# Performance work log

Measured on AMD Instinct MI355X. Metric: run time of the kernel, lower is better.

The kernel has to match this reference:

```python
import jax, jax.numpy as jnp
import numpy as np

N_HEAD = 16


def setup_inputs() -> dict:
    key = jax.random.key(0)
    ks = jax.random.split(key, 6)
    B, T, C = 2, 2048, 1024
    hs = C // N_HEAD  # 64
    block_minus_1 = 2048  # block_size - 1
    x = jax.random.normal(ks[0], (B, T, C), dtype=jnp.float32)
    W1 = jax.random.normal(ks[1], (C, C), dtype=jnp.float32) * (1.0 / np.sqrt(C))
    b1 = jnp.zeros((C,), dtype=jnp.float32)
    # original init: uniform(-1e-3, 1e-3)
    w2 = jax.random.uniform(ks[2], (hs, block_minus_1), dtype=jnp.float32, minval=-1e-3, maxval=1e-3)
    b2 = jnp.zeros((block_minus_1,), dtype=jnp.float32)
    Wv = jax.random.normal(ks[3], (C, C), dtype=jnp.float32) * (1.0 / np.sqrt(C))
    bv = jnp.zeros((C,), dtype=jnp.float32)
    Wp = jax.random.normal(ks[4], (C, C), dtype=jnp.float32) * (1.0 / np.sqrt(C))
    bp = jnp.zeros((C,), dtype=jnp.float32)
    return {"x": x, "W1": W1, "b1": b1, "w2": w2, "b2": b2,
            "Wv": Wv, "bv": bv, "Wp": Wp, "bp": bp}


def reference(x, W1, b1, w2, b2, Wv, bv, Wp, bp):
    B, T, C = x.shape
    hs = C // N_HEAD
    r = jax.nn.relu(x @ W1.T + b1).reshape(B, T, N_HEAD, hs).transpose(0, 2, 1, 3)
    # synthesizer scores: (B, nh, T, T) = relu_out @ w2[:, :T] + b2[:T]
    att = jnp.einsum('bhtd,dj->bhtj', r, w2[:, :T]) + b2[:T]
    causal = jnp.tril(jnp.ones((T, T), dtype=bool))
    att = jnp.where(causal[None, None], att, jnp.float32(-1e10))
    att = jax.nn.softmax(att, axis=-1)  # attn_drop = 0 (eval)
    v = (x @ Wv.T + bv).reshape(B, T, N_HEAD, hs).transpose(0, 2, 1, 3)
    y = jnp.einsum('bhtj,bhjd->bhtd', att, v)
    y = y.transpose(0, 2, 1, 3).reshape(B, T, C)
    return y @ Wp.T + bp  # resid_drop = 0 (eval)
```

## Files before the change

kernel.cpp:

```cpp
#include <hip/hip_runtime.h>

typedef __bf16 bf16x8 __attribute__((ext_vector_type(8)));
typedef float f32x4 __attribute__((ext_vector_type(4)));
typedef float f32x16 __attribute__((ext_vector_type(16)));

__device__ __forceinline__ unsigned short f2bf(float f) {
  union { float f; unsigned u; } v; v.f = f;
  unsigned u = v.u;
  return (unsigned short)((u + 0x7fffu + ((u >> 16) & 1u)) >> 16);
}
__device__ __forceinline__ void gload_lds16(const void* g, void* l) {
  __builtin_amdgcn_global_load_lds(
      (const __attribute__((address_space(1))) unsigned int*)g,
      (__attribute__((address_space(3))) unsigned int*)l, 16, 0, 0);
}
__device__ __forceinline__ unsigned cvtpk(float lo, float hi) {
  unsigned r;
  asm("v_cvt_pk_bf16_f32 %0, %1, %2" : "=v"(r) : "v"(lo), "v"(hi));
  return r;
}
__device__ __forceinline__ void cvt4(const float* __restrict__ s,
                                     unsigned short* __restrict__ d, int u) {
  f32x4 v = ((const f32x4*)s)[u];
  union { unsigned short s[4]; unsigned long long u; } o;
  o.s[0] = f2bf(v[0]); o.s[1] = f2bf(v[1]); o.s[2] = f2bf(v[2]); o.s[3] = f2bf(v[3]);
  ((unsigned long long*)d)[u] = o.u;
}


__global__ void prep(const float* __restrict__ x, const float* __restrict__ W1,
                     const float* __restrict__ Wv, const float* __restrict__ Wp,
                     const float* __restrict__ w2, const float* __restrict__ b2,
                     unsigned short* __restrict__ xb, unsigned short* __restrict__ W1b,
                     unsigned short* __restrict__ Wvb, unsigned short* __restrict__ Wpb,
                     unsigned short* __restrict__ w2t, unsigned short* __restrict__ ebj) {
  int u = blockIdx.x * 256 + threadIdx.x;
  if (u < 1048576) { cvt4(x, xb, u); return; }
  u -= 1048576;
  if (u < 262144) { cvt4(W1, W1b, u); return; }
  u -= 262144;
  if (u < 262144) { cvt4(Wv, Wvb, u); return; }
  u -= 262144;
  if (u < 262144) { cvt4(Wp, Wpb, u); return; }
  u -= 262144;
  if (u < 32768) {
    int j = u >> 4, d4 = (u & 15) * 4;
    union { unsigned short s[4]; unsigned long long x; } o;
#pragma unroll
    for (int i = 0; i < 4; ++i) o.s[i] = f2bf(w2[(d4 + i) * 2048 + j]);
    ((unsigned long long*)w2t)[u] = o.x;
    return;
  }
  u -= 32768;
  union { unsigned short s[4]; unsigned long long x; } o;
#pragma unroll
  for (int i = 0; i < 4; ++i) o.s[i] = f2bf(__expf(b2[u * 4 + i]));
  ((unsigned long long*)ebj)[u] = o.x;
}

__global__ __launch_bounds__(256, 3) void gemm_rv(
    const unsigned short* __restrict__ xb, const unsigned short* __restrict__ W1b,
    const unsigned short* __restrict__ Wvb, const float* __restrict__ b1,
    const float* __restrict__ bv, const float* __restrict__ b2,
    unsigned short* __restrict__ rb, unsigned short* __restrict__ vtb) {
  __shared__ unsigned short Xs[2][64 * 64];
  __shared__ unsigned short W1s[2][64 * 64];
  __shared__ unsigned short Wvs[2][64 * 64];
  const int tm = blockIdx.x * 64, n0 = blockIdx.y * 64;
  const int tid = threadIdx.x;
  const int wv = tid >> 6, ln = tid & 63;
  const int l5 = ln >> 5, l31 = ln & 31;
  const int tw = (wv & 1) * 32;
  const int cw = (wv >> 1) * 32;
  const int rowL = ln >> 3;
  const int kc = (((ln & 7) ^ rowL) & 7) * 8;

  int xoff[4], woff[4];
#pragma unroll
  for (int kk = 0; kk < 4; ++kk) {
    int c = kk * 2 + l5;
    int p = (c ^ (l31 & 7)) * 8;
    xoff[kk] = (tw + l31) * 64 + p;
    woff[kk] = (cw + l31) * 64 + p;
  }

  auto stage = [&](int k0, int bi) {
#pragma unroll
    for (int l = 0; l < 2; ++l) {
      int row = l * 32 + wv * 8 + rowL;
      gload_lds16(xb + (tm + row) * 1024 + k0 + kc, &Xs[bi][l * 2048 + wv * 512]);
      gload_lds16(W1b + (n0 + row) * 1024 + k0 + kc, &W1s[bi][l * 2048 + wv * 512]);
      gload_lds16(Wvb + (n0 + row) * 1024 + k0 + kc, &Wvs[bi][l * 2048 + wv * 512]);
    }
  };

  f32x16 accR, accV;
#pragma unroll
  for (int i = 0; i < 16; ++i) { accR[i] = 0.f; accV[i] = 0.f; }

  stage(0, 0);
  for (int it = 0; it < 16; ++it) {
    const int cb = it & 1;
    __syncthreads();
    if (it < 15) stage((it + 1) * 64, cb ^ 1);
#pragma unroll
    for (int kk = 0; kk < 4; ++kk) {
      bf16x8 xa  = *(const bf16x8*)&Xs[cb][xoff[kk]];
      bf16x8 w1f = *(const bf16x8*)&W1s[cb][woff[kk]];
      bf16x8 wvf = *(const bf16x8*)&Wvs[cb][woff[kk]];
      accR = __builtin_amdgcn_mfma_f32_32x32x16_bf16(xa, w1f, accR, 0, 0, 0);
      accV = __builtin_amdgcn_mfma_f32_32x32x16_bf16(wvf, xa, accV, 0, 0, 0);
    }
  }
  {
    int col = n0 + cw + l31;
    float bc = b1[col];
#pragma unroll
    for (int r = 0; r < 16; ++r) {
      int rr = (r & 3) + 8 * (r >> 2) + 4 * l5;
      float v = accR[r] + bc;
      rb[(tm + tw + rr) * 1024 + col] = f2bf(v > 0.f ? v : 0.f);
    }
  }
  {
    int tok = tm + tw + l31;
    float eb = __expf(b2[tok & 2047]);
#pragma unroll
    for (int r = 0; r < 16; ++r) {
      int rr = (r & 3) + 8 * (r >> 2) + 4 * l5;
      int ch = n0 + cw + rr;
      vtb[ch * 4096 + tok] = f2bf((accV[r] + bv[ch]) * eb);
    }
  }
}

__global__ __launch_bounds__(256, 4) void gemm_p(
    const unsigned short* __restrict__ A, const unsigned short* __restrict__ Bt,
    const float* __restrict__ bias, float* __restrict__ C) {
  __shared__ unsigned short As[2][64 * 64];
  __shared__ unsigned short Bs[2][64 * 64];
  const int tid = threadIdx.x;
  const int wv = tid >> 6, ln = tid & 63;
  const int l5 = ln >> 5, l31 = ln & 31;
  const int wm = (wv & 1) * 32, wn = (wv >> 1) * 32;
  const int tileM = blockIdx.y * 64, tileN = blockIdx.x * 64;
  const int rowL = ln >> 3;
  const int kc = (((ln & 7) ^ rowL) & 7) * 8;

  int aoff[4], boff[4];
#pragma unroll
  for (int kk = 0; kk < 4; ++kk) {
    int c = kk * 2 + l5;
    int p = (c ^ (l31 & 7)) * 8;
    aoff[kk] = (wm + l31) * 64 + p;
    boff[kk] = (wn + l31) * 64 + p;
  }

  auto stage = [&](int k0, int bi) {
#pragma unroll
    for (int l = 0; l < 2; ++l) {
      int row = l * 32 + wv * 8 + rowL;
      gload_lds16(A + (tileM + row) * 1024 + k0 + kc, &As[bi][l * 2048 + wv * 512]);
      gload_lds16(Bt + (tileN + row) * 1024 + k0 + kc, &Bs[bi][l * 2048 + wv * 512]);
    }
  };

  f32x16 acc;
#pragma unroll
  for (int i = 0; i < 16; ++i) acc[i] = 0.f;

  stage(0, 0);
  for (int it = 0; it < 16; ++it) {
    const int cb = it & 1;
    __syncthreads();
    if (it < 15) stage((it + 1) * 64, cb ^ 1);
#pragma unroll
    for (int kk = 0; kk < 4; ++kk) {
      bf16x8 af  = *(const bf16x8*)&As[cb][aoff[kk]];
      bf16x8 bfr = *(const bf16x8*)&Bs[cb][boff[kk]];
      acc = __builtin_amdgcn_mfma_f32_32x32x16_bf16(af, bfr, acc, 0, 0, 0);
    }
  }
#pragma unroll
  for (int r = 0; r < 16; ++r) {
    int rr = (r & 3) + 8 * (r >> 2) + 4 * l5;
    int row = tileM + wm + rr;
    int col = tileN + wn + l31;
    C[row * 1024 + col] = acc[r] + bias[col];
  }
}

__global__ __launch_bounds__(256, 2) void attn(
    const unsigned short* __restrict__ r, const unsigned short* __restrict__ w2t,
    const unsigned short* __restrict__ vt, const unsigned short* __restrict__ ebj,
    unsigned short* __restrict__ y) {
  __shared__ unsigned short W2s[2][64 * 64];
  __shared__ unsigned short Vs[2][64 * 64];

  const int tid = threadIdx.x;
  const int wv = tid >> 6, ln = tid & 63;
  const int quad = ln >> 4, lq = ln & 15;
  const int bh = blockIdx.x, b = bh >> 4, h = bh & 15;
  const int q = blockIdx.y;
  const int p = (q < 8) ? q : 23 - q;
  const int ta = p, tb = 31 - p;
  const int t0a = ta * 64, t0b = tb * 64;
  const int rowL = ln >> 3;
  const int kc = (((ln & 7) ^ rowL) & 7) * 8;
  const int sx = lq & 7;
  const int ko0 = (quad ^ sx) * 8, ko1 = ((4 + quad) ^ sx) * 8;

  bf16x8 ra[2][2];
  {
    const unsigned short* base = r + (b * 2048 + wv * 16 + lq) * 1024 + h * 64 + quad * 8;
    ra[0][0] = *(const bf16x8*)(base + t0a * 1024);
    ra[0][1] = *(const bf16x8*)(base + t0a * 1024 + 32);
    ra[1][0] = *(const bf16x8*)(base + t0b * 1024);
    ra[1][1] = *(const bf16x8*)(base + t0b * 1024 + 32);
  }

  f32x4 accY[2][4];
  f32x4 accL[2];
  const f32x4 zf = {0.f, 0.f, 0.f, 0.f};
#pragma unroll
  for (int s = 0; s < 2; ++s) {
    accL[s] = zf;
#pragma unroll
    for (int nd = 0; nd < 4; ++nd) accY[s][nd] = zf;
  }

  auto stage = [&](int jt, int bi) {
    int j0 = jt * 64;
#pragma unroll
    for (int l = 0; l < 2; ++l) {
      int row = l * 32 + wv * 8 + rowL;
      gload_lds16(w2t + (j0 + row) * 64 + kc, &W2s[bi][l * 2048 + wv * 512]);
      gload_lds16(vt + (h * 64 + row) * 4096 + b * 2048 + j0 + kc,
                  &Vs[bi][l * 2048 + wv * 512]);
    }
  };

#define TILE(S, T0, TT)                                                         \
    {                                                                           \
      f32x4 sv[4];                                                              \
      _Pragma("unroll") for (int ni = 0; ni < 4; ++ni) {                        \
        sv[ni] = __builtin_amdgcn_mfma_f32_16x16x32_bf16(w2f0[ni], ra[S][0], zf, 0, 0, 0); \
        sv[ni] = __builtin_amdgcn_mfma_f32_16x16x32_bf16(w2f1[ni], ra[S][1], sv[ni], 0, 0, 0); \
      }                                                                         \
      const bool diag = (jt == (TT));                                           \
      const int tl = (T0) + wv * 16 + lq;                                       \
      _Pragma("unroll") for (int ni = 0; ni < 4; ++ni)                          \
        _Pragma("unroll") for (int rg = 0; rg < 4; ++rg) {                      \
          float pe = __expf(sv[ni][rg]);                                        \
          if (diag) {                                                           \
            int j = j0 + ni * 16 + quad * 4 + rg;                               \
            pe = (j <= tl) ? pe : 0.f;                                          \
          }                                                                     \
          sv[ni][rg] = pe;                                                      \
        }                                                                       \
      bf16x8 pa0, pa1;                                                          \
      {                                                                         \
        union { unsigned u[4]; bf16x8 v; } k0u, k1u;                            \
        _Pragma("unroll") for (int pr = 0; pr < 2; ++pr) {                      \
          unsigned a0 = cvtpk(sv[0][2 * pr], sv[0][2 * pr + 1]);                \
          unsigned b0 = cvtpk(sv[1][2 * pr], sv[1][2 * pr + 1]);                \
          asm("v_permlane32_swap_b32 %0, %1" : "+v"(a0), "+v"(b0));             \
          asm("v_permlane16_swap_b32 %0, %1" : "+v"(a0), "+v"(b0));             \
          k0u.u[pr] = a0; k0u.u[2 + pr] = b0;                                   \
          unsigned a1 = cvtpk(sv[2][2 * pr], sv[2][2 * pr + 1]);                \
          unsigned b1 = cvtpk(sv[3][2 * pr], sv[3][2 * pr + 1]);                \
          asm("v_permlane32_swap_b32 %0, %1" : "+v"(a1), "+v"(b1));             \
          asm("v_permlane16_swap_b32 %0, %1" : "+v"(a1), "+v"(b1));             \
          k1u.u[pr] = a1; k1u.u[2 + pr] = b1;                                   \
        }                                                                       \
        pa0 = k0u.v; pa1 = k1u.v;                                               \
      }                                                                         \
      _Pragma("unroll") for (int nd = 0; nd < 4; ++nd) {                        \
        bf16x8 bb0 = *(const bf16x8*)&Vs[cb][(nd * 16 + lq) * 64 + ko0];        \
        accY[S][nd] = __builtin_amdgcn_mfma_f32_16x16x32_bf16(pa0, bb0, accY[S][nd], 0, 0, 0); \
        bf16x8 bb1 = *(const bf16x8*)&Vs[cb][(nd * 16 + lq) * 64 + ko1];        \
        accY[S][nd] = __builtin_amdgcn_mfma_f32_16x16x32_bf16(pa1, bb1, accY[S][nd], 0, 0, 0); \
      }                                                                         \
      accL[S] = __builtin_amdgcn_mfma_f32_16x16x32_bf16(pa0, eb0, accL[S], 0, 0, 0); \
      accL[S] = __builtin_amdgcn_mfma_f32_16x16x32_bf16(pa1, eb1, accL[S], 0, 0, 0); \
    }

#define WRITEOUT(S, T0)                                                         \
    {                                                                           \
      float inv[4];                                                             \
      _Pragma("unroll") for (int rg = 0; rg < 4; ++rg)                          \
        inv[rg] = __builtin_amdgcn_rcpf(accL[S][rg]);                           \
      _Pragma("unroll") for (int nd = 0; nd < 4; ++nd)                          \
        _Pragma("unroll") for (int rg = 0; rg < 4; ++rg) {                      \
          int t = (T0) + wv * 16 + quad * 4 + rg;                               \
          y[(b * 2048 + t) * 1024 + h * 64 + nd * 16 + lq] =                    \
              f2bf(accY[S][nd][rg] * inv[rg]);                                  \
        }                                                                       \
    }

  stage(0, 0);
  for (int jt = 0; jt <= tb; ++jt) {
    const int cb = jt & 1;
    __syncthreads();
    if (jt < tb) stage(jt + 1, cb ^ 1);
    const int j0 = jt * 64;

    bf16x8 eb0 = *(const bf16x8*)&ebj[j0 + quad * 8];
    bf16x8 eb1 = *(const bf16x8*)&ebj[j0 + 32 + quad * 8];
    bf16x8 w2f0[4], w2f1[4];
#pragma unroll
    for (int ni = 0; ni < 4; ++ni) {
      w2f0[ni] = *(const bf16x8*)&W2s[cb][(ni * 16 + lq) * 64 + ko0];
      w2f1[ni] = *(const bf16x8*)&W2s[cb][(ni * 16 + lq) * 64 + ko1];
    }

    if (jt <= ta) TILE(0, t0a, ta);
    TILE(1, t0b, tb);
    if (jt == ta) WRITEOUT(0, t0a);
  }
  WRITEOUT(1, t0b);
#undef TILE
#undef WRITEOUT
}

extern "C" void kernel_launch(void* const* d_in, const int* in_sizes, int n_in,
                              void* d_out, int out_size, void* d_ws, size_t ws_size,
                              hipStream_t stream) {
  const float* x  = (const float*)d_in[0];
  const float* W1 = (const float*)d_in[1];
  const float* b1 = (const float*)d_in[2];
  const float* w2 = (const float*)d_in[3];
  const float* b2 = (const float*)d_in[4];
  const float* Wv = (const float*)d_in[5];
  const float* bv = (const float*)d_in[6];
  const float* Wp = (const float*)d_in[7];
  const float* bp = (const float*)d_in[8];

  unsigned short* ws  = (unsigned short*)d_ws;
  unsigned short* xb   = ws;
  unsigned short* W1b  = ws + 4194304;
  unsigned short* Wvb  = ws + 5242880;
  unsigned short* Wpb  = ws + 6291456;
  unsigned short* w2t  = ws + 7340032;
  unsigned short* rb   = ws + 7471104;
  unsigned short* vt   = ws + 11665408;
  unsigned short* yb   = ws + 15859712;
  unsigned short* ebjb = ws + 20054016;

  prep<<<7298, 256, 0, stream>>>(x, W1, Wv, Wp, w2, b2, xb, W1b, Wvb, Wpb, w2t, ebjb);
  gemm_rv<<<dim3(64, 16), 256, 0, stream>>>(xb, W1b, Wvb, b1, bv, b2, rb, vt);
  attn<<<dim3(32, 16), 256, 0, stream>>>(rb, w2t, vt, ebjb, yb);
  gemm_p<<<dim3(16, 64), 256, 0, stream>>>(yb, Wpb, bp, (float*)d_out);
}
```

Measured before the change: 185.3 us.

## Triple-buffer LDS staging with explicit vmcnt waits in GEMM and attention kernels

Moves the GEMM and attention kernels from double-buffered LDS staging with __syncthreads to triple buffering. The prefetch now runs two tiles ahead, and each iteration waits only on its own tile through a partial s_waitcnt vmcnt plus a raw s_barrier, so one tile's loads stay in flight across the barrier. The aim is to hide more global-to-LDS latency behind the MFMA work. In exchange, LDS use per block grows and launch-bounds occupancy targets drop by one block per CU. The hand-written vmcnt counts must match the exact number of loads each stage issues.

Measured after the change: 168.7 us. -9.0%, faster.

```diff
diff --git a/kernel.cpp b/kernel.cpp
--- a/kernel.cpp
+++ b/kernel.cpp
@@ -18,6 +18,11 @@
   unsigned r;
   asm("v_cvt_pk_bf16_f32 %0, %1, %2" : "=v"(r) : "v"(lo), "v"(hi));
   return r;
+}
+template <int N> __device__ __forceinline__ void vmwait() {
+  if constexpr (N == 0) asm volatile("s_waitcnt vmcnt(0)" ::: "memory");
+  else if constexpr (N == 4) asm volatile("s_waitcnt vmcnt(4)" ::: "memory");
+  else asm volatile("s_waitcnt vmcnt(6)" ::: "memory");
 }
 __device__ __forceinline__ void cvt4(const float* __restrict__ s,
                                      unsigned short* __restrict__ d, int u) {
@@ -58,14 +63,14 @@
   ((unsigned long long*)ebj)[u] = o.x;
 }
 
-__global__ __launch_bounds__(256, 3) void gemm_rv(
+__global__ __launch_bounds__(256, 2) void gemm_rv(
     const unsigned short* __restrict__ xb, const unsigned short* __restrict__ W1b,
     const unsigned short* __restrict__ Wvb, const float* __restrict__ b1,
     const float* __restrict__ bv, const float* __restrict__ b2,
     unsigned short* __restrict__ rb, unsigned short* __restrict__ vtb) {
-  __shared__ unsigned short Xs[2][64 * 64];
-  __shared__ unsigned short W1s[2][64 * 64];
-  __shared__ unsigned short Wvs[2][64 * 64];
+  __shared__ unsigned short Xs[3][64 * 64];
+  __shared__ unsigned short W1s[3][64 * 64];
+  __shared__ unsigned short Wvs[3][64 * 64];
   const int tm = blockIdx.x * 64, n0 = blockIdx.y * 64;
   const int tid = threadIdx.x;
   const int wv = tid >> 6, ln = tid & 63;
@@ -99,10 +104,13 @@
   for (int i = 0; i < 16; ++i) { accR[i] = 0.f; accV[i] = 0.f; }
 
   stage(0, 0);
+  stage(64, 1);
   for (int it = 0; it < 16; ++it) {
-    const int cb = it & 1;
-    __syncthreads();
-    if (it < 15) stage((it + 1) * 64, cb ^ 1);
+    const int cb = it % 3;
+    if (it < 15) vmwait<6>(); else vmwait<0>();
+    __builtin_amdgcn_s_barrier();
+    __builtin_amdgcn_sched_barrier(0);
+    if (it < 14) stage((it + 2) * 64, (it + 2) % 3);
 #pragma unroll
     for (int kk = 0; kk < 4; ++kk) {
       bf16x8 xa  = *(const bf16x8*)&Xs[cb][xoff[kk]];
@@ -134,11 +142,11 @@
   }
 }
 
-__global__ __launch_bounds__(256, 4) void gemm_p(
+__global__ __launch_bounds__(256, 3) void gemm_p(
     const unsigned short* __restrict__ A, const unsigned short* __restrict__ Bt,
     const float* __restrict__ bias, float* __restrict__ C) {
-  __shared__ unsigned short As[2][64 * 64];
-  __shared__ unsigned short Bs[2][64 * 64];
+  __shared__ unsigned short As[3][64 * 64];
+  __shared__ unsigned short Bs[3][64 * 64];
   const int tid = threadIdx.x;
   const int wv = tid >> 6, ln = tid & 63;
   const int l5 = ln >> 5, l31 = ln & 31;
@@ -170,10 +178,13 @@
   for (int i = 0; i < 16; ++i) acc[i] = 0.f;
 
   stage(0, 0);
+  stage(64, 1);
   for (int it = 0; it < 16; ++it) {
-    const int cb = it & 1;
-    __syncthreads();
-    if (it < 15) stage((it + 1) * 64, cb ^ 1);
+    const int cb = it % 3;
+    if (it < 15) vmwait<4>(); else vmwait<0>();
+    __builtin_amdgcn_s_barrier();
+    __builtin_amdgcn_sched_barrier(0);
+    if (it < 14) stage((it + 2) * 64, (it + 2) % 3);
 #pragma unroll
     for (int kk = 0; kk < 4; ++kk) {
       bf16x8 af  = *(const bf16x8*)&As[cb][aoff[kk]];
@@ -194,8 +205,8 @@
     const unsigned short* __restrict__ r, const unsigned short* __restrict__ w2t,
     const unsigned short* __restrict__ vt, const unsigned short* __restrict__ ebj,
     unsigned short* __restrict__ y) {
-  __shared__ unsigned short W2s[2][64 * 64];
-  __shared__ unsigned short Vs[2][64 * 64];
+  __shared__ unsigned short W2s[3][64 * 64];
+  __shared__ unsigned short Vs[3][64 * 64];
 
   const int tid = threadIdx.x;
   const int wv = tid >> 6, ln = tid & 63;
@@ -299,10 +310,13 @@
     }
 
   stage(0, 0);
+  stage(1, 1);
   for (int jt = 0; jt <= tb; ++jt) {
-    const int cb = jt & 1;
-    __syncthreads();
-    if (jt < tb) stage(jt + 1, cb ^ 1);
+    const int cb = jt % 3;
+    if (jt < tb) vmwait<4>(); else vmwait<0>();
+    __builtin_amdgcn_s_barrier();
+    __builtin_amdgcn_sched_barrier(0);
+    if (jt + 2 <= tb) stage(jt + 2, (jt + 2) % 3);
     const int j0 = jt * 64;
 
     bf16x8 eb0 = *(const bf16x8*)&ebj[j0 + quad * 8];
```
